# Kernel optimization log

Measured on AMD Instinct MI355X. Metric: run time of the kernel, lower is better.

## Reference

```python
import jax, jax.numpy as jnp
import numpy as np
from jax import ops as jops

N = 20000          # nodes
E = 320000         # edges
IN_DIM = 16        # input_dim_features_extractor
HID = 64           # hidden_dim_features_extractor
HEADS = 4          # n_attention_heads
LAYERS = 2         # n_layers_features_extractor
NEG_SLOPE = 0.2    # DGL EGATConv leaky_relu slope


def setup_inputs() -> dict:
    key = jax.random.key(0)
    ks = jax.random.split(key, 16)
    s = lambda *sh: 1.0 / np.sqrt(sh[-2] if len(sh) >= 2 else sh[-1])
    inp = {
        "node_feat": jax.random.normal(ks[0], (N, IN_DIM), jnp.float32),
        "edge_feat": jax.random.normal(ks[1], (E, HID), jnp.float32),
        "src": jax.random.randint(ks[2], (E,), 0, N, jnp.int32),
        "dst": jax.random.randint(ks[3], (E,), 0, N, jnp.int32),
        # features_embedder (MLP n_layers=1 -> single Linear IN_DIM->HID)
        "W_embed": jax.random.normal(ks[4], (IN_DIM, HID), jnp.float32) * s(IN_DIM, HID),
        "b_embed": jnp.zeros((HID,), jnp.float32),
        # per-layer EGATConv params (stacked over layer dim)
        "W_ni": jax.random.normal(ks[5], (LAYERS, HID, HEADS * HID), jnp.float32) * s(HID, 1),
        "W_nj": jax.random.normal(ks[6], (LAYERS, HID, HEADS * HID), jnp.float32) * s(HID, 1),
        "W_fij": jax.random.normal(ks[7], (LAYERS, HID, HEADS * HID), jnp.float32) * s(HID, 1),
        "b_att": jnp.zeros((LAYERS, HEADS * HID), jnp.float32),
        "attn": jax.random.normal(ks[8], (LAYERS, HEADS, HID), jnp.float32) * s(HID),
        "W_node": jax.random.normal(ks[9], (LAYERS, HID, HEADS * HID), jnp.float32) * s(HID, 1),
        # per-layer MLP (n_layers=1 -> Linear HEADS*HID -> HID)
        "W_mlp": jax.random.normal(ks[10], (LAYERS, HEADS * HID, HID), jnp.float32) * s(HEADS * HID, 1),
        "b_mlp": jnp.zeros((LAYERS, HID), jnp.float32),
    }
    return inp


def _egat(h, f, src, dst, W_ni, W_nj, W_fij, b, attn, W_node):
    """DGL EGATConv: edge-feature attention + softmax-weighted aggregation."""
    # per-edge attention features: u_add_v + edge proj + bias
    f_ni = h @ W_ni                         # (N, H*D)
    f_nj = h @ W_nj                         # (N, H*D)
    f_fij = f @ W_fij                       # (E, H*D)
    f_out = f_ni[src] + f_nj[dst] + f_fij + b
    f_out = jax.nn.leaky_relu(f_out, NEG_SLOPE).reshape(E, HEADS, HID)
    e = jnp.einsum("ehd,hd->eh", f_out, attn)            # (E, H) logits
    # edge softmax over incoming edges of each dst node (numerically stable)
    m = jops.segment_max(e, dst, num_segments=N)          # (N, H)
    a = jnp.exp(e - m[dst])
    z = jops.segment_sum(a, dst, num_segments=N)          # (N, H)
    a = a / z[dst]
    # weighted message aggregation
    hn = (h @ W_node).reshape(N, HEADS, HID)
    msg = hn[src] * a[:, :, None]                         # (E, H, D)
    out = jops.segment_sum(msg, dst, num_segments=N)      # (N, H, D)
    return out


def reference(node_feat, edge_feat, src, dst, W_embed, b_embed,
              W_ni, W_nj, W_fij, b_att, attn, W_node, W_mlp, b_mlp):
    features_list = [node_feat]                 # layer_pooling='all'
    features = node_feat @ W_embed + b_embed    # features_embedder
    features_list.append(features)
    for L in range(LAYERS):
        h = _egat(features, edge_feat, src, dst,
                  W_ni[L], W_nj[L], W_fij[L], b_att[L], attn[L], W_node[L])
        new = h.reshape(N, HEADS * HID) @ W_mlp[L] + b_mlp[L]
        features = new + features               # residual
        features_list.append(features)
    return jnp.concatenate(features_list, axis=-1)   # (N, 16 + 3*64)
```

## Files before the change

kernel.cpp:

```cpp
#include <hip/hip_runtime.h>
#include <math.h>

#define NN 20000
#define NE 320000
#define IN_DIM 16
#define HID 64
#define HEADS 4
#define HD 256
#define OUTW 208
#define NEG 0.2f

typedef unsigned short u16;
typedef unsigned int u32;
typedef __attribute__((ext_vector_type(8))) short bf16x8;
typedef __attribute__((ext_vector_type(8))) unsigned short u16x8;
typedef __attribute__((ext_vector_type(4))) float f32x4;

__device__ __forceinline__ float b2f(u16 u) {
  union { u32 i; float f; } c; c.i = ((u32)u) << 16; return c.f;
}
__device__ __forceinline__ u16 f2b(float f) {
  union { float f; u32 i; } c; c.f = f;
  u32 r = (c.i + 0x7FFFu + ((c.i >> 16) & 1u)) >> 16;
  return (u16)r;
}

__global__ void k_embed(const float* __restrict__ nf, const float* __restrict__ We,
                        const float* __restrict__ be, float* __restrict__ feat,
                        float* __restrict__ out) {
  int tid = blockIdx.x * blockDim.x + threadIdx.x;
  int n = tid >> 6, c = tid & 63;
  if (n >= NN) return;
  float acc = be[c];
#pragma unroll
  for (int k = 0; k < IN_DIM; ++k)
    acc += nf[n * IN_DIM + k] * We[k * HID + c];
  feat[n * HID + c] = acc;
  out[n * OUTW + 16 + c] = acc;
  if (c < IN_DIM) out[n * OUTW + c] = nf[n * IN_DIM + c];
}

__global__ void k_count(const int* __restrict__ dst, int* __restrict__ counts) {
  int e = blockIdx.x * blockDim.x + threadIdx.x;
  if (e < NE) atomicAdd(&counts[dst[e]], 1);
}

__global__ void k_scan(const int* __restrict__ counts, int* __restrict__ rowptr) {
  __shared__ int wsum[16];
  __shared__ int tot;
  int lane = threadIdx.x & 63, wid = threadIdx.x >> 6;
  int running = 0;
  if (threadIdx.x == 0) rowptr[0] = 0;
  for (int base = 0; base < NN; base += 1024) {
    int i = base + threadIdx.x;
    int x = (i < NN) ? counts[i] : 0;
#pragma unroll
    for (int d = 1; d < 64; d <<= 1) {
      int t = __shfl_up(x, d);
      if (lane >= d) x += t;
    }
    if (lane == 63) wsum[wid] = x;
    __syncthreads();
    if (wid == 0) {
      int wv = (lane < 16) ? wsum[lane] : 0;
#pragma unroll
      for (int d = 1; d < 16; d <<= 1) {
        int t = __shfl_up(wv, d);
        if (lane >= d) wv += t;
      }
      if (lane < 16) wsum[lane] = wv;
      if (lane == 15) tot = wv;
    }
    __syncthreads();
    int wpre = (wid == 0) ? 0 : wsum[wid - 1];
    if (i < NN) rowptr[i + 1] = running + wpre + x;
    running += tot;
    __syncthreads();
  }
}

__global__ void k_scatter(const int* __restrict__ dst, const int* __restrict__ src,
                          const int* __restrict__ rowptr, int* __restrict__ cursor,
                          int* __restrict__ eidx, int* __restrict__ srcp,
                          int* __restrict__ dstp) {
  int e = blockIdx.x * blockDim.x + threadIdx.x;
  if (e >= NE) return;
  int d = dst[e];
  int pos = rowptr[d] + atomicAdd(&cursor[d], 1);
  eidx[pos] = e;
  srcp[pos] = src[e];
  dstp[pos] = d;
}

__global__ void k_permute(const float* __restrict__ ef, const int* __restrict__ eidx,
                          u16* __restrict__ efbp) {
  int t = blockIdx.x * blockDim.x + threadIdx.x;
  int slot = t >> 4, c = (t & 15) * 4;
  int e = eidx[slot];
  float4 v = *reinterpret_cast<const float4*>(&ef[(size_t)e * HID + c]);
  ushort4 o;
  o.x = f2b(v.x); o.y = f2b(v.y); o.z = f2b(v.z); o.w = f2b(v.w);
  *reinterpret_cast<ushort4*>(&efbp[(size_t)slot * HID + c]) = o;
}

__global__ void k_prepw(const float* __restrict__ Wf, u16* __restrict__ Wt) {
  int tid = blockIdx.x * blockDim.x + threadIdx.x;
  int n = tid >> 6, k = tid & 63;
  if (n >= HD) return;
  Wt[n * HID + k] = f2b(Wf[k * HD + n]);
}

__global__ __launch_bounds__(256) void k_nodeproj(
    const float* __restrict__ feat, const float* __restrict__ Wni,
    const float* __restrict__ Wnj, const float* __restrict__ Wnd,
    const float* __restrict__ batt, u16* __restrict__ fni,
    u16* __restrict__ fnj, u16* __restrict__ hn) {
  __shared__ float hs[8 * HID];
  int n0 = blockIdx.x * 8;
  int c = threadIdx.x;
  for (int i = threadIdx.x; i < 8 * HID; i += 256)
    hs[i] = feat[(size_t)(n0 + (i >> 6)) * HID + (i & 63)];
  __syncthreads();
  float aI[8] = {0}, aJ[8] = {0}, aN[8] = {0};
  for (int k = 0; k < HID; ++k) {
    float wi = Wni[k * HD + c], wj = Wnj[k * HD + c], wn = Wnd[k * HD + c];
#pragma unroll
    for (int t = 0; t < 8; ++t) {
      float x = hs[t * HID + k];
      aI[t] += x * wi; aJ[t] += x * wj; aN[t] += x * wn;
    }
  }
  float b = batt[c];
#pragma unroll
  for (int t = 0; t < 8; ++t) {
    int n = n0 + t;
    fni[(size_t)n * HD + c] = f2b(aI[t] + b);
    fnj[(size_t)n * HD + c] = f2b(aJ[t]);
    hn[(size_t)n * HD + c]  = f2b(aN[t]);
  }
}

__global__ __launch_bounds__(256) void k_edgelogits(
    const u16* __restrict__ efbp, const int* __restrict__ srcp,
    const int* __restrict__ dstp, const u16* __restrict__ fni,
    const u16* __restrict__ fnj, const u16* __restrict__ Wt,
    const float* __restrict__ attnL, float* __restrict__ elog) {
  __shared__ float gb[HEADS][16][68];
  int h = threadIdx.x >> 6;
  int l = threadIdx.x & 63;
  int q = l >> 4;
  int n = l & 15;
  int e0 = l >> 3;
  int cb = (l & 7) * 8;
  bf16x8 bfr[4][2];
#pragma unroll
  for (int nt = 0; nt < 4; ++nt)
#pragma unroll
    for (int kk = 0; kk < 2; ++kk)
      bfr[nt][kk] = *reinterpret_cast<const bf16x8*>(
          &Wt[(h * 64 + nt * 16 + n) * HID + kk * 32 + q * 8]);
  float at[4];
#pragma unroll
  for (int nt = 0; nt < 4; ++nt) at[nt] = attnL[h * 64 + nt * 16 + n];

#define COMMIT(av, bv, row)                                           \
  {                                                                   \
    float4 g0, g1;                                                    \
    g0.x = b2f(av[0]) + b2f(bv[0]); g0.y = b2f(av[1]) + b2f(bv[1]);   \
    g0.z = b2f(av[2]) + b2f(bv[2]); g0.w = b2f(av[3]) + b2f(bv[3]);   \
    g1.x = b2f(av[4]) + b2f(bv[4]); g1.y = b2f(av[5]) + b2f(bv[5]);   \
    g1.z = b2f(av[6]) + b2f(bv[6]); g1.w = b2f(av[7]) + b2f(bv[7]);   \
    *reinterpret_cast<float4*>(&gb[h][row][cb]) = g0;                 \
    *reinterpret_cast<float4*>(&gb[h][row][cb + 4]) = g1;             \
  }

#define TILEMMA(aa0, aa1, ibase)                                                  \
  {                                                                               \
    float sumr[4] = {0.f, 0.f, 0.f, 0.f};                                         \
    _Pragma("unroll")                                                             \
    for (int nt = 0; nt < 4; ++nt) {                                              \
      f32x4 acc = {0.f, 0.f, 0.f, 0.f};                                           \
      acc = __builtin_amdgcn_mfma_f32_16x16x32_bf16(aa0, bfr[nt][0], acc, 0, 0, 0); \
      acc = __builtin_amdgcn_mfma_f32_16x16x32_bf16(aa1, bfr[nt][1], acc, 0, 0, 0); \
      _Pragma("unroll")                                                           \
      for (int r = 0; r < 4; ++r) {                                               \
        float v = acc[r] + gb[h][q * 4 + r][nt * 16 + n];                         \
        v = v > 0.f ? v : NEG * v;                                                \
        sumr[r] += v * at[nt];                                                    \
      }                                                                           \
    }                                                                             \
    _Pragma("unroll")                                                             \
    for (int r = 0; r < 4; ++r) {                                                 \
      float v = sumr[r];                                                          \
      v += __shfl_xor(v, 1);                                                      \
      v += __shfl_xor(v, 2);                                                      \
      v += __shfl_xor(v, 4);                                                      \
      v += __shfl_xor(v, 8);                                                      \
      if (n == 0) elog[(size_t)h * NE + (ibase) + q * 4 + r] = v;                 \
    }                                                                             \
  }

  const int NT = NE / 16;
  const int G = gridDim.x;
  for (int tile = blockIdx.x; tile < NT; tile += 2 * G) {
    int t1 = tile + G;
    int i0 = tile * 16;
    bf16x8 a00 = *reinterpret_cast<const bf16x8*>(&efbp[(size_t)(i0 + n) * HID + q * 8]);
    bf16x8 a01 = *reinterpret_cast<const bf16x8*>(&efbp[(size_t)(i0 + n) * HID + 32 + q * 8]);
    int sA0 = srcp[i0 + e0],     dA0 = dstp[i0 + e0];
    int sA1 = srcp[i0 + 8 + e0], dA1 = dstp[i0 + 8 + e0];
    u16x8 avA0 = *reinterpret_cast<const u16x8*>(&fni[(size_t)sA0 * HD + h * 64 + cb]);
    u16x8 bvA0 = *reinterpret_cast<const u16x8*>(&fnj[(size_t)dA0 * HD + h * 64 + cb]);
    u16x8 avA1 = *reinterpret_cast<const u16x8*>(&fni[(size_t)sA1 * HD + h * 64 + cb]);
    u16x8 bvA1 = *reinterpret_cast<const u16x8*>(&fnj[(size_t)dA1 * HD + h * 64 + cb]);
    int i1 = 0;
    bf16x8 a10 = {}, a11 = {};
    u16x8 avB0 = {}, bvB0 = {}, avB1 = {}, bvB1 = {};
    bool has1 = (t1 < NT);
    if (has1) {
      i1 = t1 * 16;
      a10 = *reinterpret_cast<const bf16x8*>(&efbp[(size_t)(i1 + n) * HID + q * 8]);
      a11 = *reinterpret_cast<const bf16x8*>(&efbp[(size_t)(i1 + n) * HID + 32 + q * 8]);
      int sB0 = srcp[i1 + e0],     dB0 = dstp[i1 + e0];
      int sB1 = srcp[i1 + 8 + e0], dB1 = dstp[i1 + 8 + e0];
      avB0 = *reinterpret_cast<const u16x8*>(&fni[(size_t)sB0 * HD + h * 64 + cb]);
      bvB0 = *reinterpret_cast<const u16x8*>(&fnj[(size_t)dB0 * HD + h * 64 + cb]);
      avB1 = *reinterpret_cast<const u16x8*>(&fni[(size_t)sB1 * HD + h * 64 + cb]);
      bvB1 = *reinterpret_cast<const u16x8*>(&fnj[(size_t)dB1 * HD + h * 64 + cb]);
    }
    COMMIT(avA0, bvA0, e0);
    COMMIT(avA1, bvA1, 8 + e0);
    TILEMMA(a00, a01, i0);
    if (has1) {
      COMMIT(avB0, bvB0, e0);
      COMMIT(avB1, bvB1, 8 + e0);
      TILEMMA(a10, a11, i1);
    }
  }
#undef COMMIT
#undef TILEMMA
}

__global__ __launch_bounds__(256) void k_agg(
    const int* __restrict__ rowptr, const int* __restrict__ srcp,
    const float* __restrict__ elog, const u16* __restrict__ hn,
    float* __restrict__ agg) {
  int n = (blockIdx.x * blockDim.x + threadIdx.x) >> 6;
  int j = threadIdx.x & 63;
  if (n >= NN) return;
  int s0 = rowptr[n], s1 = rowptr[n + 1];
  int h = j >> 4, u = j & 15;
  const float* er = elog + (size_t)h * NE;
  float m = -1e30f;
  for (int i = s0 + u; i < s1; i += 16) m = fmaxf(m, er[i]);
  m = fmaxf(m, __shfl_xor(m, 1));
  m = fmaxf(m, __shfl_xor(m, 2));
  m = fmaxf(m, __shfl_xor(m, 4));
  m = fmaxf(m, __shfl_xor(m, 8));
  float z = 0.f;
  for (int i = s0 + u; i < s1; i += 16) z += __expf(er[i] - m);
  z += __shfl_xor(z, 1);
  z += __shfl_xor(z, 2);
  z += __shfl_xor(z, 4);
  z += __shfl_xor(z, 8);
  float invz = (z > 0.f) ? 1.0f / z : 0.f;
  float4 ac[8];
#pragma unroll
  for (int t = 0; t < 8; ++t) ac[t] = make_float4(0, 0, 0, 0);
  int i = s0;
  for (; i + 8 <= s1; i += 8) {
    int sv[8]; float wv[8]; ushort4 vv[8];
#pragma unroll
    for (int t = 0; t < 8; ++t) sv[t] = srcp[i + t];
#pragma unroll
    for (int t = 0; t < 8; ++t) wv[t] = __expf(er[i + t] - m) * invz;
#pragma unroll
    for (int t = 0; t < 8; ++t)
      vv[t] = *reinterpret_cast<const ushort4*>(&hn[(size_t)sv[t] * HD + 4 * j]);
#pragma unroll
    for (int t = 0; t < 8; ++t) {
      ac[t].x += b2f(vv[t].x) * wv[t]; ac[t].y += b2f(vv[t].y) * wv[t];
      ac[t].z += b2f(vv[t].z) * wv[t]; ac[t].w += b2f(vv[t].w) * wv[t];
    }
  }
  for (; i < s1; ++i) {
    int s = srcp[i];
    float w = __expf(er[i] - m) * invz;
    ushort4 v = *reinterpret_cast<const ushort4*>(&hn[(size_t)s * HD + 4 * j]);
    ac[0].x += b2f(v.x) * w; ac[0].y += b2f(v.y) * w;
    ac[0].z += b2f(v.z) * w; ac[0].w += b2f(v.w) * w;
  }
  float4 acc;
  acc.x = ((ac[0].x + ac[1].x) + (ac[2].x + ac[3].x)) + ((ac[4].x + ac[5].x) + (ac[6].x + ac[7].x));
  acc.y = ((ac[0].y + ac[1].y) + (ac[2].y + ac[3].y)) + ((ac[4].y + ac[5].y) + (ac[6].y + ac[7].y));
  acc.z = ((ac[0].z + ac[1].z) + (ac[2].z + ac[3].z)) + ((ac[4].z + ac[5].z) + (ac[6].z + ac[7].z));
  acc.w = ((ac[0].w + ac[1].w) + (ac[2].w + ac[3].w)) + ((ac[4].w + ac[5].w) + (ac[6].w + ac[7].w));
  *reinterpret_cast<float4*>(&agg[(size_t)n * HD + 4 * j]) = acc;
}

__global__ __launch_bounds__(256) void k_mlp(
    const float* __restrict__ agg, const float* __restrict__ Wm,
    const float* __restrict__ bm, float* __restrict__ feat,
    float* __restrict__ out, int outoff) {
  __shared__ float as_[32 * HD];
  int n0 = blockIdx.x * 32;
  for (int i = threadIdx.x; i < 32 * HD; i += 256) as_[i] = agg[(size_t)n0 * HD + i];
  __syncthreads();
  int c = threadIdx.x & 63;
  int g = threadIdx.x >> 6;
  float acc[8] = {0};
  for (int k = 0; k < HD; ++k) {
    float wv = Wm[k * HID + c];
#pragma unroll
    for (int t = 0; t < 8; ++t)
      acc[t] += as_[(g * 8 + t) * HD + k] * wv;
  }
  float b = bm[c];
#pragma unroll
  for (int t = 0; t < 8; ++t) {
    int n = n0 + g * 8 + t;
    float v = acc[t] + b + feat[n * HID + c];
    feat[n * HID + c] = v;
    out[n * OUTW + outoff + c] = v;
  }
}

extern "C" void kernel_launch(void* const* d_in, const int* in_sizes, int n_in,
                              void* d_out, int out_size, void* d_ws, size_t ws_size,
                              hipStream_t stream) {
  const float* node_feat = (const float*)d_in[0];
  const float* edge_feat = (const float*)d_in[1];
  const int*   src       = (const int*)d_in[2];
  const int*   dst       = (const int*)d_in[3];
  const float* W_embed   = (const float*)d_in[4];
  const float* b_embed   = (const float*)d_in[5];
  const float* W_ni      = (const float*)d_in[6];
  const float* W_nj      = (const float*)d_in[7];
  const float* W_fij     = (const float*)d_in[8];
  const float* b_att     = (const float*)d_in[9];
  const float* attn      = (const float*)d_in[10];
  const float* W_node    = (const float*)d_in[11];
  const float* W_mlp     = (const float*)d_in[12];
  const float* b_mlp     = (const float*)d_in[13];
  float* out = (float*)d_out;

  float* ws   = (float*)d_ws;
  float* feat = ws;
  u16*  fni   = (u16*)(feat + (size_t)NN * HID);
  u16*  fnj   = fni + (size_t)NN * HD;
  u16*  hn    = fnj + (size_t)NN * HD;
  u16*  efbp  = hn + (size_t)NN * HD;
  u16*  Wt    = efbp + (size_t)NE * HID;
  float* elog = (float*)(Wt + (size_t)HD * HID);
  int* counts = (int*)(elog + (size_t)NE * HEADS);
  int* rowptr = counts + NN;
  int* cursor = rowptr + NN + 1;
  int* eidx   = cursor + NN;
  int* srcp   = eidx + NE;
  int* dstp   = srcp + NE;
  float* aggb = (float*)fni;

  hipMemsetAsync(counts, 0, sizeof(int) * NN, stream);
  hipMemsetAsync(cursor, 0, sizeof(int) * NN, stream);

  k_embed<<<(NN * 64) / 256, 256, 0, stream>>>(node_feat, W_embed, b_embed, feat, out);
  k_count<<<NE / 256, 256, 0, stream>>>(dst, counts);
  k_scan<<<1, 1024, 0, stream>>>(counts, rowptr);
  k_scatter<<<NE / 256, 256, 0, stream>>>(dst, src, rowptr, cursor, eidx, srcp, dstp);
  k_permute<<<(NE * 16) / 256, 256, 0, stream>>>(edge_feat, eidx, efbp);

  for (int L = 0; L < 2; ++L) {
    const float* WniL = W_ni + (size_t)L * HID * HD;
    const float* WnjL = W_nj + (size_t)L * HID * HD;
    const float* WfL  = W_fij + (size_t)L * HID * HD;
    const float* WndL = W_node + (size_t)L * HID * HD;
    const float* battL = b_att + (size_t)L * HD;
    const float* attnL = attn + (size_t)L * HEADS * HID;
    const float* WmL  = W_mlp + (size_t)L * HD * HID;
    const float* bmL  = b_mlp + (size_t)L * HID;

    k_prepw<<<(HID * HD) / 256, 256, 0, stream>>>(WfL, Wt);
    k_nodeproj<<<NN / 8, 256, 0, stream>>>(feat, WniL, WnjL, WndL, battL, fni, fnj, hn);
    k_edgelogits<<<2048, 256, 0, stream>>>(efbp, srcp, dstp, fni, fnj, Wt, attnL, elog);
    k_agg<<<(NN * 64) / 256, 256, 0, stream>>>(rowptr, srcp, elog, hn, aggb);
    k_mlp<<<NN / 32, 256, 0, stream>>>(aggb, WmL, bmL, feat, out, 80 + L * 64);
  }
}
```

Measured before the change: 550.1 us.

## Add gathered node projections via identity-matrix MFMA instead of LDS staging

The edge-logit kernel no longer gathers fni/fnj rows into a shared-memory buffer and adds them per element. The gathered bf16 rows are now loaded directly in MFMA A-operand layout and accumulated into the accumulator with extra MFMAs against a constructed selection/identity B matrix. This removes LDS writes and reads and the bf16-to-float conversions, at the cost of four extra MFMAs per tile. Logit stores are also merged into a single float4 per lane group.

```diff
diff --git a/kernel.cpp b/kernel.cpp
--- a/kernel.cpp
+++ b/kernel.cpp
@@ -13,7 +13,6 @@
 typedef unsigned short u16;
 typedef unsigned int u32;
 typedef __attribute__((ext_vector_type(8))) short bf16x8;
-typedef __attribute__((ext_vector_type(8))) unsigned short u16x8;
 typedef __attribute__((ext_vector_type(4))) float f32x4;
 
 __device__ __forceinline__ float b2f(u16 u) {
@@ -145,13 +144,10 @@
     const int* __restrict__ dstp, const u16* __restrict__ fni,
     const u16* __restrict__ fnj, const u16* __restrict__ Wt,
     const float* __restrict__ attnL, float* __restrict__ elog) {
-  __shared__ float gb[HEADS][16][68];
   int h = threadIdx.x >> 6;
   int l = threadIdx.x & 63;
   int q = l >> 4;
   int n = l & 15;
-  int e0 = l >> 3;
-  int cb = (l & 7) * 8;
   bf16x8 bfr[4][2];
 #pragma unroll
   for (int nt = 0; nt < 4; ++nt)
@@ -162,19 +158,17 @@
   float at[4];
 #pragma unroll
   for (int nt = 0; nt < 4; ++nt) at[nt] = attnL[h * 64 + nt * 16 + n];
-
-#define COMMIT(av, bv, row)                                           \
-  {                                                                   \
-    float4 g0, g1;                                                    \
-    g0.x = b2f(av[0]) + b2f(bv[0]); g0.y = b2f(av[1]) + b2f(bv[1]);   \
-    g0.z = b2f(av[2]) + b2f(bv[2]); g0.w = b2f(av[3]) + b2f(bv[3]);   \
-    g1.x = b2f(av[4]) + b2f(bv[4]); g1.y = b2f(av[5]) + b2f(bv[5]);   \
-    g1.z = b2f(av[6]) + b2f(bv[6]); g1.w = b2f(av[7]) + b2f(bv[7]);   \
-    *reinterpret_cast<float4*>(&gb[h][row][cb]) = g0;                 \
-    *reinterpret_cast<float4*>(&gb[h][row][cb + 4]) = g1;             \
-  }
-
-#define TILEMMA(aa0, aa1, ibase)                                                  \
+  int tgt0 = n - 8 * q;
+  int tgt1 = 16 + n - 8 * q;
+  union { bf16x8 v; u32 w[4]; } uI0, uI1;
+#pragma unroll
+  for (int w4 = 0; w4 < 4; ++w4) {
+    uI0.w[w4] = ((2 * w4 == tgt0) ? 0x3F80u : 0u) | ((2 * w4 + 1 == tgt0) ? 0x3F800000u : 0u);
+    uI1.w[w4] = ((2 * w4 == tgt1) ? 0x3F80u : 0u) | ((2 * w4 + 1 == tgt1) ? 0x3F800000u : 0u);
+  }
+  bf16x8 bI0 = uI0.v, bI1 = uI1.v;
+
+#define TILEMMA(aa0, aa1, fi0, fi1, fj0, fj1, ibase)                              \
   {                                                                               \
     float sumr[4] = {0.f, 0.f, 0.f, 0.f};                                         \
     _Pragma("unroll")                                                             \
@@ -182,9 +176,13 @@
       f32x4 acc = {0.f, 0.f, 0.f, 0.f};                                           \
       acc = __builtin_amdgcn_mfma_f32_16x16x32_bf16(aa0, bfr[nt][0], acc, 0, 0, 0); \
       acc = __builtin_amdgcn_mfma_f32_16x16x32_bf16(aa1, bfr[nt][1], acc, 0, 0, 0); \
+      acc = __builtin_amdgcn_mfma_f32_16x16x32_bf16((nt < 2) ? fi0 : fi1,         \
+                                                    (nt & 1) ? bI1 : bI0, acc, 0, 0, 0); \
+      acc = __builtin_amdgcn_mfma_f32_16x16x32_bf16((nt < 2) ? fj0 : fj1,         \
+                                                    (nt & 1) ? bI1 : bI0, acc, 0, 0, 0); \
       _Pragma("unroll")                                                           \
       for (int r = 0; r < 4; ++r) {                                               \
-        float v = acc[r] + gb[h][q * 4 + r][nt * 16 + n];                         \
+        float v = acc[r];                                                         \
         v = v > 0.f ? v : NEG * v;                                                \
         sumr[r] += v * at[nt];                                                    \
       }                                                                           \
@@ -196,7 +194,12 @@
       v += __shfl_xor(v, 2);                                                      \
       v += __shfl_xor(v, 4);                                                      \
       v += __shfl_xor(v, 8);                                                      \
-      if (n == 0) elog[(size_t)h * NE + (ibase) + q * 4 + r] = v;                 \
+      sumr[r] = v;                                                                \
+    }                                                                             \
+    if (n == 0) {                                                                 \
+      float4 o_;                                                                  \
+      o_.x = sumr[0]; o_.y = sumr[1]; o_.z = sumr[2]; o_.w = sumr[3];             \
+      *reinterpret_cast<float4*>(&elog[(size_t)h * NE + (ibase) + q * 4]) = o_;   \
     }                                                                             \
   }
 
@@ -207,37 +210,30 @@
     int i0 = tile * 16;
     bf16x8 a00 = *reinterpret_cast<const bf16x8*>(&efbp[(size_t)(i0 + n) * HID + q * 8]);
     bf16x8 a01 = *reinterpret_cast<const bf16x8*>(&efbp[(size_t)(i0 + n) * HID + 32 + q * 8]);
-    int sA0 = srcp[i0 + e0],     dA0 = dstp[i0 + e0];
-    int sA1 = srcp[i0 + 8 + e0], dA1 = dstp[i0 + 8 + e0];
-    u16x8 avA0 = *reinterpret_cast<const u16x8*>(&fni[(size_t)sA0 * HD + h * 64 + cb]);
-    u16x8 bvA0 = *reinterpret_cast<const u16x8*>(&fnj[(size_t)dA0 * HD + h * 64 + cb]);
-    u16x8 avA1 = *reinterpret_cast<const u16x8*>(&fni[(size_t)sA1 * HD + h * 64 + cb]);
-    u16x8 bvA1 = *reinterpret_cast<const u16x8*>(&fnj[(size_t)dA1 * HD + h * 64 + cb]);
+    int sA = srcp[i0 + n], dA = dstp[i0 + n];
+    bf16x8 fiA0 = *reinterpret_cast<const bf16x8*>(&fni[(size_t)sA * HD + h * 64 + q * 8]);
+    bf16x8 fiA1 = *reinterpret_cast<const bf16x8*>(&fni[(size_t)sA * HD + h * 64 + 32 + q * 8]);
+    bf16x8 fjA0 = *reinterpret_cast<const bf16x8*>(&fnj[(size_t)dA * HD + h * 64 + q * 8]);
+    bf16x8 fjA1 = *reinterpret_cast<const bf16x8*>(&fnj[(size_t)dA * HD + h * 64 + 32 + q * 8]);
     int i1 = 0;
     bf16x8 a10 = {}, a11 = {};
-    u16x8 avB0 = {}, bvB0 = {}, avB1 = {}, bvB1 = {};
+    bf16x8 fiB0 = {}, fiB1 = {}, fjB0 = {}, fjB1 = {};
     bool has1 = (t1 < NT);
     if (has1) {
       i1 = t1 * 16;
       a10 = *reinterpret_cast<const bf16x8*>(&efbp[(size_t)(i1 + n) * HID + q * 8]);
       a11 = *reinterpret_cast<const bf16x8*>(&efbp[(size_t)(i1 + n) * HID + 32 + q * 8]);
-      int sB0 = srcp[i1 + e0],     dB0 = dstp[i1 + e0];
-      int sB1 = srcp[i1 + 8 + e0], dB1 = dstp[i1 + 8 + e0];
-      avB0 = *reinterpret_cast<const u16x8*>(&fni[(size_t)sB0 * HD + h * 64 + cb]);
-      bvB0 = *reinterpret_cast<const u16x8*>(&fnj[(size_t)dB0 * HD + h * 64 + cb]);
-      avB1 = *reinterpret_cast<const u16x8*>(&fni[(size_t)sB1 * HD + h * 64 + cb]);
-      bvB1 = *reinterpret_cast<const u16x8*>(&fnj[(size_t)dB1 * HD + h * 64 + cb]);
-    }
-    COMMIT(avA0, bvA0, e0);
-    COMMIT(avA1, bvA1, 8 + e0);
-    TILEMMA(a00, a01, i0);
+      int sB = srcp[i1 + n], dB = dstp[i1 + n];
+      fiB0 = *reinterpret_cast<const bf16x8*>(&fni[(size_t)sB * HD + h * 64 + q * 8]);
+      fiB1 = *reinterpret_cast<const bf16x8*>(&fni[(size_t)sB * HD + h * 64 + 32 + q * 8]);
+      fjB0 = *reinterpret_cast<const bf16x8*>(&fnj[(size_t)dB * HD + h * 64 + q * 8]);
+      fjB1 = *reinterpret_cast<const bf16x8*>(&fnj[(size_t)dB * HD + h * 64 + 32 + q * 8]);
+    }
+    TILEMMA(a00, a01, fiA0, fiA1, fjA0, fjA1, i0);
     if (has1) {
-      COMMIT(avB0, bvB0, e0);
-      COMMIT(avB1, bvB1, 8 + e0);
-      TILEMMA(a10, a11, i1);
-    }
-  }
-#undef COMMIT
+      TILEMMA(a10, a11, fiB0, fiB1, fjB0, fjB1, i1);
+    }
+  }
 #undef TILEMMA
 }
 
```

Result: no change. 555.5 us (+1.0%).
